# Optimization experiments

Measured on AMD Instinct MI355X. Metric: run time of the kernel, lower is better.

Reference implementation:

```python
import jax, jax.numpy as jnp
import numpy as np

B, T, IN_DIM, EMBED, OUT_DIM, WS = 32, 512, 2048, 512, 29, 64


def setup_inputs() -> dict:
    key = jax.random.key(0)
    ks = jax.random.split(key, 8)
    x = jax.random.normal(ks[0], (B, T, IN_DIM), dtype=jnp.float32)
    # pack_padded_sequence contract: lengths sorted descending, max length == T
    lens = jnp.sort(jax.random.randint(ks[1], (B,), T // 2, T + 1))[::-1]
    sample_lengths = lens.at[0].set(T).astype(jnp.int64)
    s_in = 1.0 / np.sqrt(IN_DIM)
    s_q = 1.0 / np.sqrt(OUT_DIM)
    s_o = 1.0 / np.sqrt(EMBED)
    return {
        "x": x,
        "sample_lengths": sample_lengths,
        "W_in": jax.random.normal(ks[2], (IN_DIM, EMBED), jnp.float32) * s_in,
        "b_in": jnp.zeros((EMBED,), jnp.float32),
        "W_q": jax.random.normal(ks[3], (OUT_DIM, EMBED), jnp.float32) * s_q,
        "b_q": jnp.zeros((EMBED,), jnp.float32),
        "W_out": jax.random.normal(ks[4], (EMBED, OUT_DIM), jnp.float32) * s_o,
        "b_out": jnp.zeros((OUT_DIM,), jnp.float32),
        "window_size": WS,
    }


def reference(x, sample_lengths, W_in, b_in, W_q, b_q, W_out, b_out, window_size):
    # x: [B, T, input_dim] padded (pad_packed_sequence equivalent)
    Bb, Tt, _ = x.shape
    D = W_in.shape[1]
    h = x @ W_in + b_in                       # input_proj, [B, T, D]
    lens = sample_lengths
    j = jnp.arange(Tt)
    scale = 1.0 / jnp.sqrt(jnp.asarray(D, h.dtype))
    neg = jnp.finfo(h.dtype).min
    # generate_query0 with init_strategy='fix': ones, last channel = 9
    q0 = jnp.ones((Bb, 1, W_q.shape[0]), h.dtype).at[:, :, -1].set(9.0)

    def step(query, t):
        q = query @ W_q + b_q                 # query_proj, [B, 1, D]
        scores = jnp.einsum('bod,btd->bot', q, h) * scale  # [B, 1, T]
        # local window around query index t, clipped to each sequence length
        valid = (j >= t - window_size) & (j <= t + window_size) & (j[None, :] < lens[:, None])
        w = jax.nn.softmax(jnp.where(valid[:, None, :], scores, neg), axis=-1)
        alive = (t < lens).astype(h.dtype)[:, None, None]  # finished seqs -> zeros (blank_out/blank_wgts)
        out = jnp.einsum('bot,btd->bod', w, h) * alive      # [B, 1, D]
        new_query = out @ W_out + b_out        # output_proj, [B, 1, 29]
        return new_query, (new_query[:, 0, :], (w * alive)[:, 0, :])

    _, (outs, wgts) = jax.lax.scan(step, q0, jnp.arange(Tt))
    outputs = jnp.transpose(outs, (1, 0, 2))   # [B, T, 29]
    weights = jnp.transpose(wgts, (1, 0, 2))   # [B, T, T]
    return outputs, weights
```

## Files before the change

### kernel.cpp

```cpp
#include <hip/hip_runtime.h>
#include <math.h>

#define BB 32
#define TT 512
#define IND 2048
#define DD 512
#define OD 29
#define WCOLS 64

typedef float v2f __attribute__((ext_vector_type(2)));

__device__ __forceinline__ v2f pk_fma(v2f a, v2f b, v2f c) {
  v2f d;
  asm("v_pk_fma_f32 %0, %1, %2, %3" : "=v"(d) : "v"(a), "v"(b), "v"(c));
  return d;
}

template<int CTRL, int RM>
__device__ __forceinline__ float updpp(float idv, float x) {
  return __int_as_float(__builtin_amdgcn_update_dpp(
      __float_as_int(idv), __float_as_int(x), CTRL, RM, 0xf, false));
}

__device__ __forceinline__ float red_max64(float x) {
  const float ID = -3.0e38f;
  x = fmaxf(x, updpp<0xB1, 0xf>(ID, x));
  x = fmaxf(x, updpp<0x4E, 0xf>(ID, x));
  x = fmaxf(x, updpp<0x124, 0xf>(ID, x));
  x = fmaxf(x, updpp<0x128, 0xf>(ID, x));
  x = fmaxf(x, updpp<0x142, 0xa>(ID, x));
  x = fmaxf(x, updpp<0x143, 0xc>(ID, x));
  return __int_as_float(__builtin_amdgcn_readlane(__float_as_int(x), 63));
}

__device__ __forceinline__ float red_sum64(float x) {
  x += updpp<0xB1, 0xf>(0.f, x);
  x += updpp<0x4E, 0xf>(0.f, x);
  x += updpp<0x124, 0xf>(0.f, x);
  x += updpp<0x128, 0xf>(0.f, x);
  x += updpp<0x142, 0xa>(0.f, x);
  x += updpp<0x143, 0xc>(0.f, x);
  return __int_as_float(__builtin_amdgcn_readlane(__float_as_int(x), 63));
}

__global__ void k_zero(float* __restrict__ p, int n) {
  int n4 = n >> 2;
  int i = blockIdx.x * blockDim.x + threadIdx.x;
  int stride = gridDim.x * blockDim.x;
  float4 z = make_float4(0.f, 0.f, 0.f, 0.f);
  for (int j = i; j < n4; j += stride) ((float4*)p)[j] = z;
  int base = (n4 << 2) + i;
  if (base < n) p[base] = 0.f;
}

__global__ __launch_bounds__(64) void k_transform(
    const float* __restrict__ W_in, const float* __restrict__ b_in,
    const float* __restrict__ W_q,  const float* __restrict__ b_q,
    const float* __restrict__ W_out, float* __restrict__ Wt) {
  int i = blockIdx.x;
  int c = threadIdx.x;
  const float* row = (i < IND) ? (W_in + (size_t)i * DD) : b_in;
  const float* m;
  int strd;
  bool valid = true, dscale = false;
  if (c < OD)                { m = W_q + (size_t)c * DD; strd = 1; dscale = true; }
  else if (c == OD)          { m = b_q;                  strd = 1; dscale = true; }
  else if (c >= 32 && c < 32 + OD) { m = W_out + (c - 32); strd = OD; }
  else                       { m = b_q; strd = 0; valid = false; }
  float a0 = 0.f, a1 = 0.f, a2 = 0.f, a3 = 0.f;
  for (int d = 0; d < DD; d += 4) {
    a0 += row[d + 0] * m[(size_t)(d + 0) * strd];
    a1 += row[d + 1] * m[(size_t)(d + 1) * strd];
    a2 += row[d + 2] * m[(size_t)(d + 2) * strd];
    a3 += row[d + 3] * m[(size_t)(d + 3) * strd];
  }
  float acc = (a0 + a1) + (a2 + a3);
  if (dscale) acc *= (1.0f / sqrtf((float)DD));
  if (!valid) acc = 0.f;
  Wt[(size_t)i * WCOLS + c] = acc;
}

__global__ __launch_bounds__(256) void k_gemm(
    const float* __restrict__ x, const float* __restrict__ Wt,
    float* __restrict__ GPC) {
  __shared__ float xt[128][65];
  int tid = threadIdx.x;
  int r = tid & 63;
  int cg16 = __builtin_amdgcn_readfirstlane((tid >> 6) << 4);
  int m0 = blockIdx.x << 6;
  int lr = tid >> 2, lc = tid & 3;
  const float* xl = x + (size_t)(m0 + lr) * IND;
  float4 a0 = make_float4(0,0,0,0), a1 = a0, a2 = a0, a3 = a0;
  for (int kk = 0; kk < IND; kk += 128) {
    __syncthreads();
    #pragma unroll
    for (int j = 0; j < 8; ++j) {
      int k = (lc + 4 * j) << 2;
      float4 v = *(const float4*)(xl + kk + k);
      xt[k + 0][lr] = v.x; xt[k + 1][lr] = v.y;
      xt[k + 2][lr] = v.z; xt[k + 3][lr] = v.w;
    }
    __syncthreads();
    const float* wb = Wt + (size_t)kk * WCOLS + cg16;
    #pragma unroll 4
    for (int k = 0; k < 128; ++k) {
      float xv = xt[k][r];
      const float* wk = wb + (size_t)k * WCOLS;
      float4 w0 = *(const float4*)(wk + 0);
      float4 w1 = *(const float4*)(wk + 4);
      float4 w2 = *(const float4*)(wk + 8);
      float4 w3 = *(const float4*)(wk + 12);
      a0.x += xv * w0.x; a0.y += xv * w0.y; a0.z += xv * w0.z; a0.w += xv * w0.w;
      a1.x += xv * w1.x; a1.y += xv * w1.y; a1.z += xv * w1.z; a1.w += xv * w1.w;
      a2.x += xv * w2.x; a2.y += xv * w2.y; a2.z += xv * w2.z; a2.w += xv * w2.w;
      a3.x += xv * w3.x; a3.y += xv * w3.y; a3.z += xv * w3.z; a3.w += xv * w3.w;
    }
  }
  const float* br = Wt + (size_t)IND * WCOLS + cg16;
  float4 b0 = *(const float4*)(br + 0), b1 = *(const float4*)(br + 4);
  float4 b2 = *(const float4*)(br + 8), b3 = *(const float4*)(br + 12);
  a0.x += b0.x; a0.y += b0.y; a0.z += b0.z; a0.w += b0.w;
  a1.x += b1.x; a1.y += b1.y; a1.z += b1.z; a1.w += b1.w;
  a2.x += b2.x; a2.y += b2.y; a2.z += b2.z; a2.w += b2.w;
  a3.x += b3.x; a3.y += b3.y; a3.z += b3.z; a3.w += b3.w;
  float* o = GPC + (size_t)(m0 + r) * WCOLS + cg16;
  *(float4*)(o + 0) = a0; *(float4*)(o + 4)  = a1;
  *(float4*)(o + 8) = a2; *(float4*)(o + 12) = a3;
}

__device__ __forceinline__ void ld_g(v2f* g, const float* gb, int j) {
  const float4* s = (const float4*)(gb + (size_t)j * WCOLS);
  #pragma unroll
  for (int u = 0; u < 8; ++u) {
    float4 v = s[u];
    g[2*u+0] = (v2f){v.x, v.y};
    g[2*u+1] = (v2f){v.z, v.w};
  }
}

__device__ __forceinline__ float score_pk(const v2f* g, const v2f* qp) {
  v2f a0 = pk_fma(qp[0], g[0], (v2f){0.f, 0.f});
  v2f a1 = pk_fma(qp[1], g[1], (v2f){0.f, 0.f});
  v2f a2 = pk_fma(qp[2], g[2], (v2f){0.f, 0.f});
  #pragma unroll
  for (int i = 3; i < 15; i += 3) {
    a0 = pk_fma(qp[i+0], g[i+0], a0);
    a1 = pk_fma(qp[i+1], g[i+1], a1);
    a2 = pk_fma(qp[i+2], g[i+2], a2);
  }
  v2f s = a0 + a1;
  s = s + a2;
  return s.x + s.y;
}

__global__ __launch_bounds__(64, 1) void k_scan(
    const float* __restrict__ GPC, const int* __restrict__ lens_raw,
    const float* __restrict__ b_out, const int* __restrict__ wsp,
    float* __restrict__ outputs, float* __restrict__ weights) {
  __shared__ __align__(16) float Pt[OD * TT];
  __shared__ __align__(16) float w_lds[640];

  int b = blockIdx.x;
  int l = threadIdx.x;
  int len;
  {
    int probe = lens_raw[1];
    len = (probe == 0) ? lens_raw[2 * b] : lens_raw[b];
  }
  if (len > TT) len = TT;
  if (len < 0) len = 0;
  int ws = wsp[0];

  const float* gb = GPC + (size_t)b * TT * WCOLS;
  for (int j0 = 0; j0 < TT; j0 += 64) {
    int j = j0 + l;
    int j4 = j >> 2, jm = j & 3;
    const float* src = gb + (size_t)j * WCOLS + 32;
    #pragma unroll
    for (int u = 0; u < 8; ++u) {
      float4 v = *(const float4*)(src + 4 * u);
      int kb = 4 * u;
      if (kb + 0 < OD) Pt[(kb+0)*TT + (((j4 + kb+0) & 127) << 2) + jm] = v.x;
      if (kb + 1 < OD) Pt[(kb+1)*TT + (((j4 + kb+1) & 127) << 2) + jm] = v.y;
      if (kb + 2 < OD) Pt[(kb+2)*TT + (((j4 + kb+2) & 127) << 2) + jm] = v.z;
      if (kb + 3 < OD) Pt[(kb+3)*TT + (((j4 + kb+3) & 127) << 2) + jm] = v.w;
    }
  }
  for (int j = l; j < 640; j += 64) w_lds[j] = 0.f;
  __syncthreads();

  int k = l & 31, h = l >> 5;
  float boutk = (k < OD) ? b_out[k] : 0.f;

  float* outb = outputs + (size_t)b * TT * OD;
  float* wb   = weights + (size_t)b * TT * TT;

  v2f qp[15];
  #pragma unroll
  for (int i = 0; i < 14; ++i) qp[i] = (v2f){1.f, 1.f};
  qp[14] = (v2f){9.f, 1.f};

  v2f g0[16], g1[16], g2[16];
  int j0r = l, j1r = 64 + l, j2r = 128 + l;
  ld_g(g0, gb, j0r); ld_g(g1, gb, j1r); ld_g(g2, gb, j2r);

  int jlo = 0;
  int jhi = (ws < len - 1) ? ws : (len - 1);

  float m_run = -3.0e38f;
  int t = 0;
  for (; t < len; ++t) {
    float s0 = score_pk(g0, qp);
    float s1 = score_pk(g1, qp);
    float s2 = score_pk(g2, qp);
    bool v0 = (j0r >= jlo) & (j0r <= jhi);
    bool v1 = (j1r >= jlo) & (j1r <= jhi);
    bool v2 = (j2r >= jlo) & (j2r <= jhi);
    const float NEG = -3.0e38f;
    float mx0 = fmaxf(fmaxf(v0 ? s0 : NEG, v1 ? s1 : NEG), v2 ? s2 : NEG);
    float mx;
    if (__all(mx0 <= m_run + 8.0f) && __any(mx0 >= m_run - 20.0f)) {
      mx = m_run;
    } else {
      mx = red_max64(mx0);
      m_run = mx;
    }
    float e0 = v0 ? __expf(s0 - mx) : 0.f;
    float e1 = v1 ? __expf(s1 - mx) : 0.f;
    float e2 = v2 ? __expf(s2 - mx) : 0.f;
    if (l == 0 && jlo > 0) w_lds[jlo - 1] = 0.f;
    if (v0) w_lds[j0r] = e0;
    if (v1) w_lds[j1r] = e1;
    if (v2) w_lds[j2r] = e2;
    int jnew = t + 1 + ws;
    if (jnew >= 192 && jnew < TT) {
      int sl = (jnew >> 6) % 3;
      int ln = jnew & 63;
      if (sl == 0)      { if (l == ln) { ld_g(g0, gb, jnew); j0r = jnew; } }
      else if (sl == 1) { if (l == ln) { ld_g(g1, gb, jnew); j1r = jnew; } }
      else              { if (l == ln) { ld_g(g2, gb, jnew); j2r = jnew; } }
    }
    float sm = red_sum64(e0 + e1 + e2);
    float invS = __builtin_amdgcn_rcpf(sm);
    v2f p01 = (v2f){0.f, 0.f}, p23 = (v2f){0.f, 0.f};
    int qlo = jlo >> 2;
    if (k < OD) {
      const float* pr = Pt + k * TT;
      #pragma unroll
      for (int i = 0; i < 17; ++i) {
        int qq = qlo + h + (i << 1);
        float4 wv = *(const float4*)(w_lds + (qq << 2));
        float4 pv = *(const float4*)(pr + (((qq + k) & 127) << 2));
        p01 = pk_fma((v2f){wv.x, wv.y}, (v2f){pv.x, pv.y}, p01);
        p23 = pk_fma((v2f){wv.z, wv.w}, (v2f){pv.z, pv.w}, p23);
      }
    }
    float tot = (p01.x + p01.y) + (p23.x + p23.y);
    tot += __shfl_xor(tot, 32);
    float nq = tot * invS + boutk;
    if (h == 0 && k < OD) outb[(size_t)t * OD + k] = nq;
    float* wrow = wb + (size_t)t * TT;
    if (v0) wrow[j0r == t + 1 + ws ? -1 + 1 + j0r - 1 : j0r] = e0 * invS;
    if (v1) wrow[j1r] = e1 * invS;
    if (v2) wrow[j2r] = e2 * invS;
    #pragma unroll
    for (int kk = 0; kk < 14; ++kk) {
      float lo = __int_as_float(__builtin_amdgcn_readlane(__float_as_int(nq), 2*kk));
      float hi = __int_as_float(__builtin_amdgcn_readlane(__float_as_int(nq), 2*kk+1));
      qp[kk] = (v2f){lo, hi};
    }
    qp[14] = (v2f){__int_as_float(__builtin_amdgcn_readlane(__float_as_int(nq), 28)), 1.0f};
    jlo = (t + 1) - ws; if (jlo < 0) jlo = 0;
    jhi = (t + 1) + ws; if (jhi > len - 1) jhi = len - 1;
  }
  for (; t < TT; ++t)
    if (l < OD) outb[(size_t)t * OD + l] = boutk;
}

extern "C" void kernel_launch(void* const* d_in, const int* in_sizes, int n_in,
                              void* d_out, int out_size, void* d_ws, size_t ws_size,
                              hipStream_t stream) {
  const float* x     = (const float*)d_in[0];
  const int*   lens  = (const int*)d_in[1];
  const float* W_in  = (const float*)d_in[2];
  const float* b_in  = (const float*)d_in[3];
  const float* W_q   = (const float*)d_in[4];
  const float* b_q   = (const float*)d_in[5];
  const float* W_out = (const float*)d_in[6];
  const float* b_out = (const float*)d_in[7];
  const int*   wsp   = (const int*)d_in[8];
  float* out = (float*)d_out;

  float* Wt  = (float*)d_ws;
  float* GPC = Wt + (size_t)(IND + 1) * WCOLS;

  k_zero<<<1024, 256, 0, stream>>>(out, out_size);
  k_transform<<<IND + 1, 64, 0, stream>>>(W_in, b_in, W_q, b_q, W_out, Wt);
  k_gemm<<<(BB * TT) / 64, 256, 0, stream>>>(x, Wt, GPC);

  float* outputs = out;
  float* weights = out + (size_t)BB * TT * OD;
  k_scan<<<BB, 64, 0, stream>>>(GPC, lens, b_out, wsp, outputs, weights);
}
```

Measured before the change: 932.2 us.

## Speculate softmax exps, prefetch window rows earlier, use padded Pt layout

Computes the exponentials against the running max before the uniformity check, and recomputes them only on the rare rescale path. This takes the vote and branch off the critical path of the serial time step. The next window row is now fetched after the weighted-sum and store phase and one step earlier (t+2+ws), so global-load latency overlaps more of the loop. The swizzled Pt layout is replaced by a padded row stride of 516, which simplifies address arithmetic in the inner dot loop, possibly at the cost of some LDS bank conflicts.

```diff
diff --git a/kernel.cpp b/kernel.cpp
--- a/kernel.cpp
+++ b/kernel.cpp
@@ -7,6 +7,7 @@
 #define DD 512
 #define OD 29
 #define WCOLS 64
+#define PTS 516
 
 typedef float v2f __attribute__((ext_vector_type(2)));
 
@@ -157,7 +158,7 @@
     const float* __restrict__ GPC, const int* __restrict__ lens_raw,
     const float* __restrict__ b_out, const int* __restrict__ wsp,
     float* __restrict__ outputs, float* __restrict__ weights) {
-  __shared__ __align__(16) float Pt[OD * TT];
+  __shared__ __align__(16) float Pt[OD * PTS];
   __shared__ __align__(16) float w_lds[640];
 
   int b = blockIdx.x;
@@ -174,16 +175,15 @@
   const float* gb = GPC + (size_t)b * TT * WCOLS;
   for (int j0 = 0; j0 < TT; j0 += 64) {
     int j = j0 + l;
-    int j4 = j >> 2, jm = j & 3;
     const float* src = gb + (size_t)j * WCOLS + 32;
     #pragma unroll
     for (int u = 0; u < 8; ++u) {
       float4 v = *(const float4*)(src + 4 * u);
       int kb = 4 * u;
-      if (kb + 0 < OD) Pt[(kb+0)*TT + (((j4 + kb+0) & 127) << 2) + jm] = v.x;
-      if (kb + 1 < OD) Pt[(kb+1)*TT + (((j4 + kb+1) & 127) << 2) + jm] = v.y;
-      if (kb + 2 < OD) Pt[(kb+2)*TT + (((j4 + kb+2) & 127) << 2) + jm] = v.z;
-      if (kb + 3 < OD) Pt[(kb+3)*TT + (((j4 + kb+3) & 127) << 2) + jm] = v.w;
+      if (kb + 0 < OD) Pt[(kb+0)*PTS + j] = v.x;
+      if (kb + 1 < OD) Pt[(kb+1)*PTS + j] = v.y;
+      if (kb + 2 < OD) Pt[(kb+2)*PTS + j] = v.z;
+      if (kb + 3 < OD) Pt[(kb+3)*PTS + j] = v.w;
     }
   }
   for (int j = l; j < 640; j += 64) w_lds[j] = 0.f;
@@ -218,21 +218,45 @@
     bool v2 = (j2r >= jlo) & (j2r <= jhi);
     const float NEG = -3.0e38f;
     float mx0 = fmaxf(fmaxf(v0 ? s0 : NEG, v1 ? s1 : NEG), v2 ? s2 : NEG);
-    float mx;
-    if (__all(mx0 <= m_run + 8.0f) && __any(mx0 >= m_run - 20.0f)) {
-      mx = m_run;
-    } else {
-      mx = red_max64(mx0);
-      m_run = mx;
-    }
+    float mx = m_run;
     float e0 = v0 ? __expf(s0 - mx) : 0.f;
     float e1 = v1 ? __expf(s1 - mx) : 0.f;
     float e2 = v2 ? __expf(s2 - mx) : 0.f;
+    if (!(__all(mx0 <= m_run + 8.0f) && __any(mx0 >= m_run - 20.0f))) {
+      mx = red_max64(mx0);
+      m_run = mx;
+      e0 = v0 ? __expf(s0 - mx) : 0.f;
+      e1 = v1 ? __expf(s1 - mx) : 0.f;
+      e2 = v2 ? __expf(s2 - mx) : 0.f;
+    }
     if (l == 0 && jlo > 0) w_lds[jlo - 1] = 0.f;
     if (v0) w_lds[j0r] = e0;
     if (v1) w_lds[j1r] = e1;
     if (v2) w_lds[j2r] = e2;
-    int jnew = t + 1 + ws;
+    float sm = red_sum64(e0 + e1 + e2);
+    float invS = __builtin_amdgcn_rcpf(sm);
+    v2f p01 = (v2f){0.f, 0.f}, p23 = (v2f){0.f, 0.f};
+    int qlo = jlo >> 2;
+    if (k < OD) {
+      const float* pr = Pt + k * PTS + ((qlo + h) << 2);
+      const float* wr = w_lds + ((qlo + h) << 2);
+      #pragma unroll
+      for (int i = 0; i < 17; ++i) {
+        float4 wv = *(const float4*)(wr + (i << 3));
+        float4 pv = *(const float4*)(pr + (i << 3));
+        p01 = pk_fma((v2f){wv.x, wv.y}, (v2f){pv.x, pv.y}, p01);
+        p23 = pk_fma((v2f){wv.z, wv.w}, (v2f){pv.z, pv.w}, p23);
+      }
+    }
+    float tot = (p01.x + p01.y) + (p23.x + p23.y);
+    tot += __shfl_xor(tot, 32);
+    float nq = tot * invS + boutk;
+    if (h == 0 && k < OD) outb[(size_t)t * OD + k] = nq;
+    float* wrow = wb + (size_t)t * TT;
+    if (v0) wrow[j0r] = e0 * invS;
+    if (v1) wrow[j1r] = e1 * invS;
+    if (v2) wrow[j2r] = e2 * invS;
+    int jnew = t + 2 + ws;
     if (jnew >= 192 && jnew < TT) {
       int sl = (jnew >> 6) % 3;
       int ln = jnew & 63;
@@ -240,29 +264,6 @@
       else if (sl == 1) { if (l == ln) { ld_g(g1, gb, jnew); j1r = jnew; } }
       else              { if (l == ln) { ld_g(g2, gb, jnew); j2r = jnew; } }
     }
-    float sm = red_sum64(e0 + e1 + e2);
-    float invS = __builtin_amdgcn_rcpf(sm);
-    v2f p01 = (v2f){0.f, 0.f}, p23 = (v2f){0.f, 0.f};
-    int qlo = jlo >> 2;
-    if (k < OD) {
-      const float* pr = Pt + k * TT;
-      #pragma unroll
-      for (int i = 0; i < 17; ++i) {
-        int qq = qlo + h + (i << 1);
-        float4 wv = *(const float4*)(w_lds + (qq << 2));
-        float4 pv = *(const float4*)(pr + (((qq + k) & 127) << 2));
-        p01 = pk_fma((v2f){wv.x, wv.y}, (v2f){pv.x, pv.y}, p01);
-        p23 = pk_fma((v2f){wv.z, wv.w}, (v2f){pv.z, pv.w}, p23);
-      }
-    }
-    float tot = (p01.x + p01.y) + (p23.x + p23.y);
-    tot += __shfl_xor(tot, 32);
-    float nq = tot * invS + boutk;
-    if (h == 0 && k < OD) outb[(size_t)t * OD + k] = nq;
-    float* wrow = wb + (size_t)t * TT;
-    if (v0) wrow[j0r == t + 1 + ws ? -1 + 1 + j0r - 1 : j0r] = e0 * invS;
-    if (v1) wrow[j1r] = e1 * invS;
-    if (v2) wrow[j2r] = e2 * invS;
     #pragma unroll
     for (int kk = 0; kk < 14; ++kk) {
       float lo = __int_as_float(__builtin_amdgcn_readlane(__float_as_int(nq), 2*kk));
```

Result: faster. 883.9 us (-5.2%).
